# Kernel tuning notes

Measured on AMD Instinct MI355X. Metric: run time of the kernel, lower is better.

## Reference

```python
import jax, jax.numpy as jnp
import numpy as np

N_NODES = 100000
N_EDGES = 800000
D_IN = 512
D_OUT = 512


def setup_inputs() -> dict:
    key = jax.random.key(0)
    ks = jax.random.split(key, 6)
    std = 1.0 / np.sqrt(D_OUT)
    return {
        "x": jax.random.normal(ks[0], (N_NODES, D_IN), dtype=jnp.float32),
        "adj_row": jax.random.randint(ks[1], (N_EDGES,), 0, N_NODES, dtype=jnp.int32),
        "adj_col": jax.random.randint(ks[2], (N_EDGES,), 0, N_NODES, dtype=jnp.int32),
        "adj_vals": jax.random.uniform(ks[3], (N_EDGES,), dtype=jnp.float32),
        "weight": jax.random.uniform(ks[4], (D_IN, D_OUT), minval=-std, maxval=std, dtype=jnp.float32),
        "b": jax.random.uniform(ks[5], (D_OUT,), minval=-std, maxval=std, dtype=jnp.float32),
    }


def reference(x, adj_row, adj_col, adj_vals, weight, b):
    # support = X W  : dense GEMM [N, D_in] x [D_in, D_out]
    support = jnp.matmul(x, weight)
    # output = A @ support + b, A given as COO (row, col, vals)
    gathered = adj_vals[:, None] * support[adj_col]  # [E, D_out]
    out = jax.ops.segment_sum(gathered, adj_row, num_segments=N_NODES)
    return out + b
```

## Files before the change

kernel.cpp:

```cpp
#include <hip/hip_runtime.h>
#include <hip/hip_bf16.h>
#include <stdint.h>

#define D 512
#define D4 (D / 4)
#define SB 256

typedef __bf16 bf16x8 __attribute__((ext_vector_type(8)));
typedef float  f32x4  __attribute__((ext_vector_type(4)));

__device__ __forceinline__ unsigned short f2bf(float f) {
    uint32_t u = __float_as_uint(f);
    uint32_t r = u + 0x7fffu + ((u >> 16) & 1u);
    return (unsigned short)(r >> 16);
}

__device__ __forceinline__ uint32_t pack2(float lo, float hi) {
    return (uint32_t)f2bf(lo) | ((uint32_t)f2bf(hi) << 16);
}

__global__ __launch_bounds__(256) void cvt_x_kernel(const float4* __restrict__ x,
                                                    uint4* __restrict__ xb,
                                                    long n8) {
    long i = (long)blockIdx.x * 256 + threadIdx.x;
    if (i >= n8) return;
    float4 a = x[i * 2];
    float4 b = x[i * 2 + 1];
    uint4 o;
    o.x = pack2(a.x, a.y);
    o.y = pack2(a.z, a.w);
    o.z = pack2(b.x, b.y);
    o.w = pack2(b.z, b.w);
    xb[i] = o;
}

__global__ __launch_bounds__(256) void cvt_w_kernel(const float* __restrict__ w,
                                                    unsigned short* __restrict__ wt) {
    __shared__ float t[32][33];
    const int tx = threadIdx.x & 31;
    const int ty = threadIdx.x >> 5;
    const int n0 = blockIdx.x * 32;
    const int k0 = blockIdx.y * 32;
#pragma unroll
    for (int i = 0; i < 4; ++i)
        t[ty + i * 8][tx] = w[(long)(k0 + ty + i * 8) * D + n0 + tx];
    __syncthreads();
#pragma unroll
    for (int i = 0; i < 4; ++i)
        wt[(long)(n0 + ty + i * 8) * D + k0 + tx] = f2bf(t[tx][ty + i * 8]);
}

__global__ __launch_bounds__(256) void zero_kernel(int* __restrict__ p, int n) {
    int i = blockIdx.x * 256 + threadIdx.x;
    if (i < n) p[i] = 0;
}

__global__ __launch_bounds__(256) void hist_kernel(const int* __restrict__ erow,
                                                   int* __restrict__ cnt, int nE) {
    int i = blockIdx.x * 256 + threadIdx.x;
    int stride = gridDim.x * 256;
    for (; i < nE; i += stride) atomicAdd(&cnt[erow[i]], 1);
}

__global__ __launch_bounds__(256) void scan_part_kernel(const int* __restrict__ cnt,
                                                        int* __restrict__ bsum, int M) {
    const int b = blockIdx.x;
    const int chunk = (M + SB - 1) / SB;
    const int lo = b * chunk;
    const int hi = min(M, lo + chunk);
    int s = 0;
    for (int i = lo + (int)threadIdx.x; i < hi; i += 256) s += cnt[i];
#pragma unroll
    for (int off = 32; off; off >>= 1) s += __shfl_down(s, off);
    __shared__ int ws[4];
    const int wv = threadIdx.x >> 6;
    if ((threadIdx.x & 63) == 0) ws[wv] = s;
    __syncthreads();
    if (threadIdx.x == 0) bsum[b] = ws[0] + ws[1] + ws[2] + ws[3];
}

__global__ __launch_bounds__(SB) void scan_base_kernel(const int* __restrict__ bsum,
                                                       int* __restrict__ bbase,
                                                       int* __restrict__ rowptr, int M) {
    const int tid  = (int)threadIdx.x;
    const int lane = tid & 63;
    const int wv   = tid >> 6;
    const int v = bsum[tid];
    int s = v;
#pragma unroll
    for (int off = 1; off < 64; off <<= 1) {
        int t = __shfl_up(s, off);
        if (lane >= off) s += t;
    }
    __shared__ int wsum[4];
    if (lane == 63) wsum[wv] = s;
    __syncthreads();
    int wb = 0;
    for (int j = 0; j < wv; ++j) wb += wsum[j];
    bbase[tid] = wb + s - v;
    if (tid == SB - 1) rowptr[M] = wb + s;
}

__global__ __launch_bounds__(256) void scan_final_kernel(const int* __restrict__ cnt,
                                                         const int* __restrict__ bbase,
                                                         int* __restrict__ rowptr,
                                                         int* __restrict__ heads, int M) {
    const int b = blockIdx.x;
    const int chunk = (M + SB - 1) / SB;
    const int lo = b * chunk;
    const int hi = min(M, lo + chunk);
    const int lane = threadIdx.x & 63;
    const int wv   = threadIdx.x >> 6;
    __shared__ int wsum[4];
    __shared__ int s_carry;
    if (threadIdx.x == 0) s_carry = bbase[b];
    __syncthreads();
    for (int base = lo; base < hi; base += 256) {
        const int i = base + (int)threadIdx.x;
        const int v = (i < hi) ? cnt[i] : 0;
        int s = v;
#pragma unroll
        for (int off = 1; off < 64; off <<= 1) {
            int t = __shfl_up(s, off);
            if (lane >= off) s += t;
        }
        if (lane == 63) wsum[wv] = s;
        __syncthreads();
        int wb = s_carry;
        for (int j = 0; j < wv; ++j) wb += wsum[j];
        const int excl = wb + s - v;
        if (i < hi) { rowptr[i] = excl; heads[i] = excl; }
        __syncthreads();
        if (threadIdx.x == 0) s_carry += wsum[0] + wsum[1] + wsum[2] + wsum[3];
        __syncthreads();
    }
}

__global__ __launch_bounds__(256) void edge_sort_kernel(const int* __restrict__ erow,
                                                        const int* __restrict__ ecol,
                                                        const float* __restrict__ eval,
                                                        int* __restrict__ heads,
                                                        int* __restrict__ scol,
                                                        float* __restrict__ sval,
                                                        int nE) {
    int i = blockIdx.x * 256 + threadIdx.x;
    int stride = gridDim.x * 256;
    for (; i < nE; i += stride) {
        const int r = erow[i];
        const int p = atomicAdd(&heads[r], 1);
        scol[p] = ecol[i];
        sval[p] = eval[i];
    }
}

__global__ __launch_bounds__(256) void gemm_kernel(const unsigned short* __restrict__ Xb,
                                                   const unsigned short* __restrict__ Wt,
                                                   unsigned short* __restrict__ Sup,
                                                   int M) {
    __shared__ __align__(16) unsigned short As[128 * 64];
    __shared__ __align__(16) unsigned short Bs[128 * 64];
    const int tid  = threadIdx.x;
    const int wv   = tid >> 6;
    const int lane = tid & 63;
    const int tileM = blockIdx.x * 128;
    const int tileN = blockIdx.y * 128;
    const int wm = wv >> 1, wn = wv & 1;

    f32x4 acc[4][4];
#pragma unroll
    for (int i = 0; i < 4; ++i)
#pragma unroll
        for (int j = 0; j < 4; ++j) acc[i][j] = (f32x4)0.0f;

    const int srow = lane >> 3;
    const int sgrn = (lane & 7) ^ srow;
    const int scol = sgrn * 8;

    const int fm  = lane & 15;
    const int fkq = lane >> 4;

    for (int kt = 0; kt < D; kt += 64) {
        __syncthreads();
#pragma unroll
        for (int i = 0; i < 4; ++i) {
            const int c   = wv * 4 + i;
            const int row = c * 8 + srow;
            int rg = tileM + row;
            rg = (rg < M) ? rg : (M - 1);
            const unsigned short* ga = Xb + (long)rg * D + kt + scol;
            __builtin_amdgcn_global_load_lds(
                (const __attribute__((address_space(1))) void*)ga,
                (__attribute__((address_space(3))) void*)(As + c * 512), 16, 0, 0);
            const unsigned short* gb = Wt + (long)(tileN + row) * D + kt + scol;
            __builtin_amdgcn_global_load_lds(
                (const __attribute__((address_space(1))) void*)gb,
                (__attribute__((address_space(3))) void*)(Bs + c * 512), 16, 0, 0);
        }
        __syncthreads();
#pragma unroll
        for (int kk = 0; kk < 2; ++kk) {
            bf16x8 af[4], bfr[4];
#pragma unroll
            for (int mi = 0; mi < 4; ++mi) {
                const int m = wm * 64 + mi * 16 + fm;
                const int g = (kk * 4 + fkq) ^ (m & 7);
                af[mi] = *(const bf16x8*)(As + m * 64 + g * 8);
            }
#pragma unroll
            for (int ni = 0; ni < 4; ++ni) {
                const int n = wn * 64 + ni * 16 + fm;
                const int g = (kk * 4 + fkq) ^ (n & 7);
                bfr[ni] = *(const bf16x8*)(Bs + n * 64 + g * 8);
            }
#pragma unroll
            for (int mi = 0; mi < 4; ++mi)
#pragma unroll
                for (int ni = 0; ni < 4; ++ni)
                    acc[mi][ni] = __builtin_amdgcn_mfma_f32_16x16x32_bf16(
                        af[mi], bfr[ni], acc[mi][ni], 0, 0, 0);
        }
    }

    const int colb = tileN + wn * 64 + fm;
#pragma unroll
    for (int mi = 0; mi < 4; ++mi) {
        const int rb = tileM + wm * 64 + mi * 16 + fkq * 4;
#pragma unroll
        for (int r = 0; r < 4; ++r) {
            const int row = rb + r;
            if (row < M) {
                unsigned short* dst = Sup + (long)row * D + colb;
#pragma unroll
                for (int ni = 0; ni < 4; ++ni)
                    dst[ni * 16] = f2bf(acc[mi][ni][r]);
            }
        }
    }
}

__global__ __launch_bounds__(256) void aggregate_kernel(const unsigned short* __restrict__ sup,
                                                        const int* __restrict__ rowptr,
                                                        const int* __restrict__ scol,
                                                        const float* __restrict__ sval,
                                                        const float* __restrict__ bias,
                                                        float* __restrict__ out,
                                                        int M) {
    const int lane = threadIdx.x & 63;
    const int row  = (int)((blockIdx.x * 256 + threadIdx.x) >> 6);
    if (row >= M) return;
    int e = rowptr[row];
    const int end = rowptr[row + 1];

    const float4 b0 = ((const float4*)bias)[lane * 2];
    const float4 b1 = ((const float4*)bias)[lane * 2 + 1];
    float acc[8] = {b0.x, b0.y, b0.z, b0.w, b1.x, b1.y, b1.z, b1.w};

    for (; e + 4 <= end; e += 4) {
        const int c0 = scol[e + 0], c1 = scol[e + 1];
        const int c2 = scol[e + 2], c3 = scol[e + 3];
        const float v0 = sval[e + 0], v1 = sval[e + 1];
        const float v2 = sval[e + 2], v3 = sval[e + 3];
        const uint4 p0 = *(const uint4*)(sup + (long)c0 * D + lane * 8);
        const uint4 p1 = *(const uint4*)(sup + (long)c1 * D + lane * 8);
        const uint4 p2 = *(const uint4*)(sup + (long)c2 * D + lane * 8);
        const uint4 p3 = *(const uint4*)(sup + (long)c3 * D + lane * 8);
        const uint32_t pk0[4] = {p0.x, p0.y, p0.z, p0.w};
        const uint32_t pk1[4] = {p1.x, p1.y, p1.z, p1.w};
        const uint32_t pk2[4] = {p2.x, p2.y, p2.z, p2.w};
        const uint32_t pk3[4] = {p3.x, p3.y, p3.z, p3.w};
#pragma unroll
        for (int i = 0; i < 4; ++i) {
            acc[i * 2]     += v0 * __uint_as_float((pk0[i] & 0x0000ffffu) << 16);
            acc[i * 2 + 1] += v0 * __uint_as_float(pk0[i] & 0xffff0000u);
            acc[i * 2]     += v1 * __uint_as_float((pk1[i] & 0x0000ffffu) << 16);
            acc[i * 2 + 1] += v1 * __uint_as_float(pk1[i] & 0xffff0000u);
            acc[i * 2]     += v2 * __uint_as_float((pk2[i] & 0x0000ffffu) << 16);
            acc[i * 2 + 1] += v2 * __uint_as_float(pk2[i] & 0xffff0000u);
            acc[i * 2]     += v3 * __uint_as_float((pk3[i] & 0x0000ffffu) << 16);
            acc[i * 2 + 1] += v3 * __uint_as_float(pk3[i] & 0xffff0000u);
        }
    }
    for (; e + 2 <= end; e += 2) {
        const int c0 = scol[e + 0], c1 = scol[e + 1];
        const float v0 = sval[e + 0], v1 = sval[e + 1];
        const uint4 p0 = *(const uint4*)(sup + (long)c0 * D + lane * 8);
        const uint4 p1 = *(const uint4*)(sup + (long)c1 * D + lane * 8);
        const uint32_t pk0[4] = {p0.x, p0.y, p0.z, p0.w};
        const uint32_t pk1[4] = {p1.x, p1.y, p1.z, p1.w};
#pragma unroll
        for (int i = 0; i < 4; ++i) {
            acc[i * 2]     += v0 * __uint_as_float((pk0[i] & 0x0000ffffu) << 16);
            acc[i * 2 + 1] += v0 * __uint_as_float(pk0[i] & 0xffff0000u);
            acc[i * 2]     += v1 * __uint_as_float((pk1[i] & 0x0000ffffu) << 16);
            acc[i * 2 + 1] += v1 * __uint_as_float(pk1[i] & 0xffff0000u);
        }
    }
    for (; e < end; ++e) {
        const int c   = scol[e];
        const float v = sval[e];
        const uint4 p = *(const uint4*)(sup + (long)c * D + lane * 8);
        const uint32_t pk[4] = {p.x, p.y, p.z, p.w};
#pragma unroll
        for (int i = 0; i < 4; ++i) {
            acc[i * 2]     += v * __uint_as_float((pk[i] & 0x0000ffffu) << 16);
            acc[i * 2 + 1] += v * __uint_as_float(pk[i] & 0xffff0000u);
        }
    }

    f32x4* dst = (f32x4*)(out + (long)row * D);
    f32x4 o0 = {acc[0], acc[1], acc[2], acc[3]};
    f32x4 o1 = {acc[4], acc[5], acc[6], acc[7]};
    __builtin_nontemporal_store(o0, dst + lane * 2);
    __builtin_nontemporal_store(o1, dst + lane * 2 + 1);
}

extern "C" void kernel_launch(void* const* d_in, const int* in_sizes, int n_in,
                              void* d_out, int out_size, void* d_ws, size_t ws_size,
                              hipStream_t stream) {
    const float* x        = (const float*)d_in[0];
    const int*   adj_row  = (const int*)d_in[1];
    const int*   adj_col  = (const int*)d_in[2];
    const float* adj_vals = (const float*)d_in[3];
    const float* weight   = (const float*)d_in[4];
    const float* bias     = (const float*)d_in[5];
    float* out = (float*)d_out;

    const int M = in_sizes[0] / D;
    const int E = in_sizes[1];

    char* ws = (char*)d_ws;
    size_t off = 0;
    unsigned short* Xb  = (unsigned short*)(ws + off); off += (size_t)M * D * 2;
    unsigned short* Sup = (unsigned short*)(ws + off); off += (size_t)M * D * 2;
    unsigned short* Wt  = (unsigned short*)(ws + off); off += (size_t)D * D * 2;
    int*   rowptr = (int*)(ws + off);   off += (size_t)(M + 1) * 4;
    int*   heads  = (int*)(ws + off);   off += (size_t)M * 4;
    int*   scol   = (int*)(ws + off);   off += (size_t)E * 4;
    float* sval   = (float*)(ws + off); off += (size_t)E * 4;
    int*   bsum   = (int*)(ws + off);   off += (size_t)SB * 4;
    int*   bbase  = (int*)(ws + off);   off += (size_t)SB * 4;
    int* cnt = heads;

    zero_kernel<<<(M + 255) / 256, 256, 0, stream>>>(cnt, M);
    hist_kernel<<<1024, 256, 0, stream>>>(adj_row, cnt, E);
    scan_part_kernel<<<SB, 256, 0, stream>>>(cnt, bsum, M);
    scan_base_kernel<<<1, SB, 0, stream>>>(bsum, bbase, rowptr, M);
    scan_final_kernel<<<SB, 256, 0, stream>>>(cnt, bbase, rowptr, heads, M);
    edge_sort_kernel<<<1024, 256, 0, stream>>>(adj_row, adj_col, adj_vals,
                                               heads, scol, sval, E);

    {
        long n8 = (long)M * D / 8;
        cvt_x_kernel<<<(int)((n8 + 255) / 256), 256, 0, stream>>>(
            (const float4*)x, (uint4*)Xb, n8);
    }
    cvt_w_kernel<<<dim3(D / 32, D / 32), 256, 0, stream>>>(weight, Wt);
    gemm_kernel<<<dim3((M + 127) / 128, D / 128), 256, 0, stream>>>(Xb, Wt, Sup, M);

    aggregate_kernel<<<(M * 64 + 255) / 256, 256, 0, stream>>>(
        Sup, rowptr, scol, sval, bias, out, M);
}
```

Baseline: 656.8 us.

## Split aggregation into two column-half passes to shrink gather working set

The aggregation kernel now handles only 256 of the 512 output columns per launch, with each lane loading 4 bf16 values (8 bytes) per edge instead of 8, and it is launched twice with column offsets 0 and 256. Each pass touches only half of every support row, so the gathered working set (about 51 MB per half) is more likely to stay in the last-level cache. The cost is reading the CSR row pointers, columns and values twice, running twice as many wavefronts with narrower loads, and using plain stores in place of nontemporal stores.

```diff
diff --git a/kernel.cpp b/kernel.cpp
--- a/kernel.cpp
+++ b/kernel.cpp
@@ -5,6 +5,7 @@
 #define D 512
 #define D4 (D / 4)
 #define SB 256
+#define CHUNK 256
 
 typedef __bf16 bf16x8 __attribute__((ext_vector_type(8)));
 typedef float  f32x4  __attribute__((ext_vector_type(4)));
@@ -17,6 +18,13 @@
 
 __device__ __forceinline__ uint32_t pack2(float lo, float hi) {
     return (uint32_t)f2bf(lo) | ((uint32_t)f2bf(hi) << 16);
+}
+
+__device__ __forceinline__ float bflo(uint32_t p) {
+    return __uint_as_float((p & 0x0000ffffu) << 16);
+}
+__device__ __forceinline__ float bfhi(uint32_t p) {
+    return __uint_as_float(p & 0xffff0000u);
 }
 
 __global__ __launch_bounds__(256) void cvt_x_kernel(const float4* __restrict__ x,
@@ -244,74 +252,56 @@
                                                         const float* __restrict__ sval,
                                                         const float* __restrict__ bias,
                                                         float* __restrict__ out,
-                                                        int M) {
+                                                        int M, int c0) {
     const int lane = threadIdx.x & 63;
     const int row  = (int)((blockIdx.x * 256 + threadIdx.x) >> 6);
     if (row >= M) return;
     int e = rowptr[row];
     const int end = rowptr[row + 1];
 
-    const float4 b0 = ((const float4*)bias)[lane * 2];
-    const float4 b1 = ((const float4*)bias)[lane * 2 + 1];
-    float acc[8] = {b0.x, b0.y, b0.z, b0.w, b1.x, b1.y, b1.z, b1.w};
+    const float4 b0 = *(const float4*)(bias + c0 + lane * 4);
+    float acc[4] = {b0.x, b0.y, b0.z, b0.w};
+
+    const unsigned short* supc = sup + c0 + lane * 4;
 
     for (; e + 4 <= end; e += 4) {
-        const int c0 = scol[e + 0], c1 = scol[e + 1];
-        const int c2 = scol[e + 2], c3 = scol[e + 3];
+        const int cc0 = scol[e + 0], cc1 = scol[e + 1];
+        const int cc2 = scol[e + 2], cc3 = scol[e + 3];
         const float v0 = sval[e + 0], v1 = sval[e + 1];
         const float v2 = sval[e + 2], v3 = sval[e + 3];
-        const uint4 p0 = *(const uint4*)(sup + (long)c0 * D + lane * 8);
-        const uint4 p1 = *(const uint4*)(sup + (long)c1 * D + lane * 8);
-        const uint4 p2 = *(const uint4*)(sup + (long)c2 * D + lane * 8);
-        const uint4 p3 = *(const uint4*)(sup + (long)c3 * D + lane * 8);
-        const uint32_t pk0[4] = {p0.x, p0.y, p0.z, p0.w};
-        const uint32_t pk1[4] = {p1.x, p1.y, p1.z, p1.w};
-        const uint32_t pk2[4] = {p2.x, p2.y, p2.z, p2.w};
-        const uint32_t pk3[4] = {p3.x, p3.y, p3.z, p3.w};
-#pragma unroll
-        for (int i = 0; i < 4; ++i) {
-            acc[i * 2]     += v0 * __uint_as_float((pk0[i] & 0x0000ffffu) << 16);
-            acc[i * 2 + 1] += v0 * __uint_as_float(pk0[i] & 0xffff0000u);
-            acc[i * 2]     += v1 * __uint_as_float((pk1[i] & 0x0000ffffu) << 16);
-            acc[i * 2 + 1] += v1 * __uint_as_float(pk1[i] & 0xffff0000u);
-            acc[i * 2]     += v2 * __uint_as_float((pk2[i] & 0x0000ffffu) << 16);
-            acc[i * 2 + 1] += v2 * __uint_as_float(pk2[i] & 0xffff0000u);
-            acc[i * 2]     += v3 * __uint_as_float((pk3[i] & 0x0000ffffu) << 16);
-            acc[i * 2 + 1] += v3 * __uint_as_float(pk3[i] & 0xffff0000u);
-        }
+        const uint2 p0 = *(const uint2*)(supc + (long)cc0 * D);
+        const uint2 p1 = *(const uint2*)(supc + (long)cc1 * D);
+        const uint2 p2 = *(const uint2*)(supc + (long)cc2 * D);
+        const uint2 p3 = *(const uint2*)(supc + (long)cc3 * D);
+        acc[0] += v0 * bflo(p0.x); acc[1] += v0 * bfhi(p0.x);
+        acc[2] += v0 * bflo(p0.y); acc[3] += v0 * bfhi(p0.y);
+        acc[0] += v1 * bflo(p1.x); acc[1] += v1 * bfhi(p1.x);
+        acc[2] += v1 * bflo(p1.y); acc[3] += v1 * bfhi(p1.y);
+        acc[0] += v2 * bflo(p2.x); acc[1] += v2 * bfhi(p2.x);
+        acc[2] += v2 * bflo(p2.y); acc[3] += v2 * bfhi(p2.y);
+        acc[0] += v3 * bflo(p3.x); acc[1] += v3 * bfhi(p3.x);
+        acc[2] += v3 * bflo(p3.y); acc[3] += v3 * bfhi(p3.y);
     }
     for (; e + 2 <= end; e += 2) {
-        const int c0 = scol[e + 0], c1 = scol[e + 1];
+        const int cc0 = scol[e + 0], cc1 = scol[e + 1];
         const float v0 = sval[e + 0], v1 = sval[e + 1];
-        const uint4 p0 = *(const uint4*)(sup + (long)c0 * D + lane * 8);
-        const uint4 p1 = *(const uint4*)(sup + (long)c1 * D + lane * 8);
-        const uint32_t pk0[4] = {p0.x, p0.y, p0.z, p0.w};
-        const uint32_t pk1[4] = {p1.x, p1.y, p1.z, p1.w};
-#pragma unroll
-        for (int i = 0; i < 4; ++i) {
-            acc[i * 2]     += v0 * __uint_as_float((pk0[i] & 0x0000ffffu) << 16);
-            acc[i * 2 + 1] += v0 * __uint_as_float(pk0[i] & 0xffff0000u);
-            acc[i * 2]     += v1 * __uint_as_float((pk1[i] & 0x0000ffffu) << 16);
-            acc[i * 2 + 1] += v1 * __uint_as_float(pk1[i] & 0xffff0000u);
-        }
+        const uint2 p0 = *(const uint2*)(supc + (long)cc0 * D);
+        const uint2 p1 = *(const uint2*)(supc + (long)cc1 * D);
+        acc[0] += v0 * bflo(p0.x); acc[1] += v0 * bfhi(p0.x);
+        acc[2] += v0 * bflo(p0.y); acc[3] += v0 * bfhi(p0.y);
+        acc[0] += v1 * bflo(p1.x); acc[1] += v1 * bfhi(p1.x);
+        acc[2] += v1 * bflo(p1.y); acc[3] += v1 * bfhi(p1.y);
     }
     for (; e < end; ++e) {
-        const int c   = scol[e];
+        const int cc = scol[e];
         const float v = sval[e];
-        const uint4 p = *(const uint4*)(sup + (long)c * D + lane * 8);
-        const uint32_t pk[4] = {p.x, p.y, p.z, p.w};
-#pragma unroll
-        for (int i = 0; i < 4; ++i) {
-            acc[i * 2]     += v * __uint_as_float((pk[i] & 0x0000ffffu) << 16);
-            acc[i * 2 + 1] += v * __uint_as_float(pk[i] & 0xffff0000u);
-        }
-    }
-
-    f32x4* dst = (f32x4*)(out + (long)row * D);
-    f32x4 o0 = {acc[0], acc[1], acc[2], acc[3]};
-    f32x4 o1 = {acc[4], acc[5], acc[6], acc[7]};
-    __builtin_nontemporal_store(o0, dst + lane * 2);
-    __builtin_nontemporal_store(o1, dst + lane * 2 + 1);
+        const uint2 p = *(const uint2*)(supc + (long)cc * D);
+        acc[0] += v * bflo(p.x); acc[1] += v * bfhi(p.x);
+        acc[2] += v * bflo(p.y); acc[3] += v * bfhi(p.y);
+    }
+
+    *(float4*)(out + (long)row * D + c0 + lane * 4) =
+        (float4){acc[0], acc[1], acc[2], acc[3]};
 }
 
 extern "C" void kernel_launch(void* const* d_in, const int* in_sizes, int n_in,
@@ -358,5 +348,7 @@
     gemm_kernel<<<dim3((M + 127) / 128, D / 128), 256, 0, stream>>>(Xb, Wt, Sup, M);
 
     aggregate_kernel<<<(M * 64 + 255) / 256, 256, 0, stream>>>(
-        Sup, rowptr, scol, sval, bias, out, M);
-}
+        Sup, rowptr, scol, sval, bias, out, M, 0);
+    aggregate_kernel<<<(M * 64 + 255) / 256, 256, 0, stream>>>(
+        Sup, rowptr, scol, sval, bias, out, M, CHUNK);
+}
```

Result: no change. 649.0 us (-1.2%).
